# Optimization experiments

Measured on AMD Instinct MI355X. Metric: run time of the kernel, lower is better.

## Reference

```python
import jax, jax.numpy as jnp
import numpy as np

EMBED_DIM = 1024
NUM_HEADS = 16
HEAD_DIM = EMBED_DIM // NUM_HEADS
MAX_LEN = 1000  # default in RelativePositionalEncoding
B, T = 4, 1024


def setup_inputs() -> dict:
    key = jax.random.key(0)
    ks = jax.random.split(key, 12)
    s = 0.02
    d = EMBED_DIM
    return {
        "query": jax.random.normal(ks[0], (B, T, d), jnp.float32),
        "key": jax.random.normal(ks[1], (B, T, d), jnp.float32),
        "value": jax.random.normal(ks[2], (B, T, d), jnp.float32),
        "Wq": jax.random.normal(ks[3], (d, d), jnp.float32) * s,
        "bq": jnp.zeros((d,), jnp.float32),
        "Wk": jax.random.normal(ks[4], (d, d), jnp.float32) * s,
        "bk": jnp.zeros((d,), jnp.float32),
        "Wv": jax.random.normal(ks[5], (d, d), jnp.float32) * s,
        "bv": jnp.zeros((d,), jnp.float32),
        "Wo": jax.random.normal(ks[6], (d, d), jnp.float32) * s,
        "bo": jnp.zeros((d,), jnp.float32),
        "rel_emb": jax.random.normal(ks[7], (2 * MAX_LEN - 1, HEAD_DIM), jnp.float32) * s,
    }


def reference(query, key, value, Wq, bq, Wk, bk, Wv, bv, Wo, bo, rel_emb):
    Bq, Tq, C = query.shape
    H, hd = NUM_HEADS, HEAD_DIM
    # projections -> [B, H, T, hd]
    q = (query @ Wq.T + bq).reshape(Bq, Tq, H, hd).transpose(0, 2, 1, 3)
    k = (key @ Wk.T + bk).reshape(Bq, Tq, H, hd).transpose(0, 2, 1, 3)
    v = (value @ Wv.T + bv).reshape(Bq, Tq, H, hd).transpose(0, 2, 1, 3)
    # content scores [B, H, T, T]
    attn_scores = jnp.einsum('bhtd,bhsd->bhts', q, k)
    # relative positional embedding gather: E[t, s] = rel_emb[clamp(s - t + max_len - 1)]
    pos = jnp.arange(Tq)
    idx = jnp.clip(pos[None, :] - pos[:, None] + MAX_LEN - 1, 0, 2 * MAX_LEN - 2)
    E = rel_emb[idx]  # [T, T, hd]
    # NOTE: original uses raw (unprojected) query reshaped into heads for rel-pos scores
    rpe_q = query.transpose(1, 0, 2).reshape(Tq, Bq * H, hd)  # [T, B*H, hd]
    rpe = jnp.einsum('tnd,tsd->nts', rpe_q, E).reshape(Bq, H, Tq, Tq)
    # faithful to original: divide by scale = hd**-0.5 (i.e. multiply by sqrt(hd))
    scale = hd ** (-0.5)
    attn = (attn_scores + rpe) / scale
    attn_weights = jax.nn.softmax(attn, axis=-1)
    out = jnp.einsum('bhts,bhsd->bhtd', attn_weights, v)
    out = out.transpose(0, 2, 1, 3).reshape(Bq, Tq, C)
    return out @ Wo.T + bo
```

## Files before the change

kernel.cpp:

```cpp
#include <hip/hip_runtime.h>
#include <math.h>

typedef _Float16 h16;
typedef __attribute__((ext_vector_type(4))) _Float16 half4;
typedef __attribute__((ext_vector_type(8))) _Float16 half8;
typedef __attribute__((ext_vector_type(4))) float f32x4;

#define AS1 __attribute__((address_space(1)))
#define AS3 __attribute__((address_space(3)))
#define MFMA16(a, b, c) __builtin_amdgcn_mfma_f32_16x16x32_f16((a), (b), (c), 0, 0, 0)

__device__ __forceinline__ float ex2(float x) {
  return __builtin_amdgcn_exp2f(x);
}

__global__ __launch_bounds__(256) void convert(
    const float* __restrict__ q, const float* __restrict__ k,
    const float* __restrict__ v, const float* __restrict__ Wq,
    const float* __restrict__ Wk, const float* __restrict__ Wv,
    const float* __restrict__ Wo, const float* __restrict__ rel, h16* q16c,
    h16* k16c, h16* v16c, h16* Wq16, h16* Wk16, h16* Wv16, h16* Wo16,
    h16* relb) {
  const int i = blockIdx.x * 256 + threadIdx.x;
  if (i >= 4226304) return;
  const float* src;
  h16* dst;
  int off;
  if (i < 1048576) {
    src = q; dst = q16c; off = i;
  } else if (i < 2097152) {
    src = k; dst = k16c; off = i - 1048576;
  } else if (i < 3145728) {
    src = v; dst = v16c; off = i - 2097152;
  } else if (i < 3407872) {
    src = Wq; dst = Wq16; off = i - 3145728;
  } else if (i < 3670016) {
    src = Wk; dst = Wk16; off = i - 3407872;
  } else if (i < 3932160) {
    src = Wv; dst = Wv16; off = i - 3670016;
  } else if (i < 4194304) {
    src = Wo; dst = Wo16; off = i - 3932160;
  } else {
    off = i - 4194304;
    half4 hv = (half4){(h16)0.f, (h16)0.f, (h16)0.f, (h16)0.f};
    if (off < 31984) {
      float4 f = *(const float4*)(rel + (size_t)off * 4);
      hv = (half4){(h16)f.x, (h16)f.y, (h16)f.z, (h16)f.w};
    }
    *(half4*)(relb + (size_t)off * 4) = hv;
    return;
  }
  float4 f = *(const float4*)(src + (size_t)off * 4);
  *(half4*)(dst + (size_t)off * 4) =
      (half4){(h16)f.x, (h16)f.y, (h16)f.z, (h16)f.w};
}

template <int MODE>
__device__ __forceinline__ void gemm128_body(const h16* __restrict__ A,
                                             const h16* __restrict__ Bt,
                                             const float* __restrict__ bias,
                                             h16* __restrict__ outp) {
  __shared__ alignas(16) h16 As[128 * 32];
  __shared__ alignas(16) h16 Bs[128 * 32];
  const int tid = threadIdx.x;
  const int wave = tid >> 6;
  const int lane = tid & 63;
  const int wm = wave >> 1, wn = wave & 1;
  const int tm0 = blockIdx.x * 128, tn0 = blockIdx.y * 128;
  const int lrow = lane & 15;
  const int kq = lane >> 4;
  const int srow = lane >> 2;
  const int scol = (lane & 3) * 8;

  f32x4 acc[4][4];
#pragma unroll
  for (int i = 0; i < 4; ++i)
#pragma unroll
    for (int j = 0; j < 4; ++j) acc[i][j] = (f32x4){0.f, 0.f, 0.f, 0.f};

  for (int k0 = 0; k0 < 1024; k0 += 32) {
    __syncthreads();
#pragma unroll
    for (int rep = 0; rep < 2; ++rep) {
      const int cw = wave * 2 + rep;
      const int row = cw * 16 + srow;
      __builtin_amdgcn_global_load_lds(
          (const AS1 void*)(A + (size_t)(tm0 + row) * 1024 + k0 + scol),
          (AS3 void*)(As + cw * 512), 16, 0, 0);
      __builtin_amdgcn_global_load_lds(
          (const AS1 void*)(Bt + (size_t)(tn0 + row) * 1024 + k0 + scol),
          (AS3 void*)(Bs + cw * 512), 16, 0, 0);
    }
    __syncthreads();
    half8 af[4], bf[4];
#pragma unroll
    for (int i = 0; i < 4; ++i)
      af[i] = *(const half8*)(As + (wm * 64 + i * 16 + lrow) * 32 + kq * 8);
#pragma unroll
    for (int j = 0; j < 4; ++j)
      bf[j] = *(const half8*)(Bs + (wn * 64 + j * 16 + lrow) * 32 + kq * 8);
#pragma unroll
    for (int i = 0; i < 4; ++i)
#pragma unroll
      for (int j = 0; j < 4; ++j) acc[i][j] = MFMA16(af[i], bf[j], acc[i][j]);
  }

#pragma unroll
  for (int j = 0; j < 4; ++j) {
    const int n = tn0 + wn * 64 + j * 16 + lrow;
    const float bval = bias[n];
#pragma unroll
    for (int i = 0; i < 4; ++i) {
      const int rowb = wm * 64 + i * 16 + kq * 4;
#pragma unroll
      for (int r = 0; r < 4; ++r) {
        const int m = tm0 + rowb + r;
        const float val = acc[i][j][r] + bval;
        const int b = m >> 10, t = m & 1023, hh = n >> 6, d = n & 63;
        if (MODE == 0) {
          outp[((size_t)((b << 4) + hh) << 16) + (t << 6) + d] = (h16)val;
        } else {
          outp[(((size_t)((b << 4) + hh) * 64 + d) << 10) + t] = (h16)val;
        }
      }
    }
  }
}

__global__ __launch_bounds__(256) void qkv_gemm(
    const h16* q16c, const h16* k16c, const h16* v16c, const h16* Wq16,
    const h16* Wk16, const h16* Wv16, const float* bq, const float* bk,
    const float* bv, h16* q16, h16* k16, h16* vt16) {
  const int z = blockIdx.z;
  const h16* A = (z == 0) ? q16c : (z == 1) ? k16c : v16c;
  const h16* Bt = (z == 0) ? Wq16 : (z == 1) ? Wk16 : Wv16;
  const float* bias = (z == 0) ? bq : (z == 1) ? bk : bv;
  if (z == 2)
    gemm128_body<1>(A, Bt, bias, vt16);
  else
    gemm128_body<0>(A, Bt, bias, (z == 0) ? q16 : k16);
}

__global__ __launch_bounds__(256) void out_gemm(const h16* __restrict__ A,
                                                const h16* __restrict__ Bt,
                                                const float* __restrict__ bo,
                                                float* __restrict__ out) {
  __shared__ alignas(16) h16 As[64 * 32];
  __shared__ alignas(16) h16 Bs[128 * 32];
  const int tid = threadIdx.x;
  const int wave = tid >> 6;
  const int lane = tid & 63;
  const int wm = wave >> 1, wn = wave & 1;
  const int tm0 = blockIdx.x * 64, tn0 = blockIdx.y * 128;
  const int lrow = lane & 15;
  const int kq = lane >> 4;
  const int srow = lane >> 2;
  const int scol = (lane & 3) * 8;

  f32x4 acc[2][4];
#pragma unroll
  for (int i = 0; i < 2; ++i)
#pragma unroll
    for (int j = 0; j < 4; ++j) acc[i][j] = (f32x4){0.f, 0.f, 0.f, 0.f};

  for (int k0 = 0; k0 < 1024; k0 += 32) {
    __syncthreads();
    {
      const int row = wave * 16 + srow;
      __builtin_amdgcn_global_load_lds(
          (const AS1 void*)(A + (size_t)(tm0 + row) * 1024 + k0 + scol),
          (AS3 void*)(As + wave * 512), 16, 0, 0);
    }
#pragma unroll
    for (int rep = 0; rep < 2; ++rep) {
      const int cw = wave * 2 + rep;
      const int row = cw * 16 + srow;
      __builtin_amdgcn_global_load_lds(
          (const AS1 void*)(Bt + (size_t)(tn0 + row) * 1024 + k0 + scol),
          (AS3 void*)(Bs + cw * 512), 16, 0, 0);
    }
    __syncthreads();
    half8 af[2], bf[4];
#pragma unroll
    for (int i = 0; i < 2; ++i)
      af[i] = *(const half8*)(As + (wm * 32 + i * 16 + lrow) * 32 + kq * 8);
#pragma unroll
    for (int j = 0; j < 4; ++j)
      bf[j] = *(const half8*)(Bs + (wn * 64 + j * 16 + lrow) * 32 + kq * 8);
#pragma unroll
    for (int i = 0; i < 2; ++i)
#pragma unroll
      for (int j = 0; j < 4; ++j) acc[i][j] = MFMA16(af[i], bf[j], acc[i][j]);
  }

#pragma unroll
  for (int j = 0; j < 4; ++j) {
    const int n = tn0 + wn * 64 + j * 16 + lrow;
    const float bval = bo[n];
#pragma unroll
    for (int i = 0; i < 2; ++i) {
      const int rowb = wm * 32 + i * 16 + kq * 4;
#pragma unroll
      for (int r = 0; r < 4; ++r) {
        const int m = tm0 + rowb + r;
        out[(size_t)m * 1024 + n] = acc[i][j][r] + bval;
      }
    }
  }
}

__global__ __launch_bounds__(256, 4) void attn_mfma(
    const h16* __restrict__ q16, const h16* __restrict__ k16,
    const h16* __restrict__ vt16, const h16* __restrict__ q16c,
    const h16* __restrict__ relb, h16* __restrict__ ao) {
  __shared__ alignas(16) h16 Kh[4096];
  __shared__ alignas(16) h16 Rl[8192];
  __shared__ alignas(16) h16 VtS[4096];
  __shared__ alignas(16) h16 Ps[4096];

  const int bid = blockIdx.x;
  const int ttile = bid & 15;
  const int bh = bid >> 4;
  const int b = bh >> 4, h = bh & 15;
  const int t0 = ttile << 6;
  const int tid = threadIdx.x;
  const int w = tid >> 6;
  const int lane = tid & 63;
  const int l15 = lane & 15;
  const int kq = lane >> 4;

  const int tq = t0 + w * 16 + l15;
  half8 aq[2], arq[2];
#pragma unroll
  for (int ks = 0; ks < 2; ++ks) {
    aq[ks] =
        *(const half8*)(q16 + ((size_t)bh * 1024 + tq) * 64 + kq * 8 + ks * 32);
    arq[ks] = *(const half8*)(q16c + ((size_t)(b * 1024 + tq)) * 1024 + h * 64 +
                              kq * 8 + ks * 32);
  }

  float m2[4], ls[4];
  f32x4 O[4];
#pragma unroll
  for (int r = 0; r < 4; ++r) {
    m2[r] = -1e30f;
    ls[r] = 0.f;
  }
#pragma unroll
  for (int db = 0; db < 4; ++db) O[db] = (f32x4){0.f, 0.f, 0.f, 0.f};

  const int trow = w * 16 + kq * 4;

  for (int s0 = 0; s0 < 1024; s0 += 64) {
    __syncthreads();
    for (int i = tid; i < 512; i += 256) {
      const int row = i >> 3, c = i & 7;
      *(half8*)(Kh + row * 64 + ((c ^ (row & 7)) << 3)) = *(const half8*)(
          k16 + ((size_t)(bh * 1024 + s0 + row)) * 64 + c * 8);
    }
    for (int i = tid; i < 512; i += 256) {
      const int row = i >> 3, c = i & 7;
      *(half8*)(VtS + row * 64 + ((c ^ (row & 7)) << 3)) = *(const half8*)(
          vt16 + ((size_t)bh * 64 + row) * 1024 + s0 + c * 8);
    }
    const int base = s0 - t0 + 999 - 63;
    for (int i = tid; i < 1024; i += 256) {
      const int row = i >> 3, c = i & 7;
      int ridx = base + row;
      ridx = ridx < 0 ? 0 : (ridx > 1998 ? 1998 : ridx);
      *(half8*)(Rl + row * 64 + ((c ^ (row & 7)) << 3)) =
          *(const half8*)(relb + (size_t)ridx * 64 + c * 8);
    }
    __syncthreads();

    f32x4 S[4];
#pragma unroll
    for (int ns = 0; ns < 4; ++ns) {
      f32x4 s = (f32x4){0.f, 0.f, 0.f, 0.f};
      const int kr = ns * 16 + l15;
#pragma unroll
      for (int ks = 0; ks < 2; ++ks) {
        const int c = ((ks * 4 + kq) ^ (kr & 7)) << 3;
        s = MFMA16(aq[ks], *(const half8*)(Kh + kr * 64 + c), s);
      }
      S[ns] = s;
    }

    f32x4 G[5];
#pragma unroll
    for (int gi = 0; gi < 5; ++gi) {
      f32x4 g = (f32x4){0.f, 0.f, 0.f, 0.f};
      const int ur = (3 - w + gi) * 16 + l15;
#pragma unroll
      for (int ks = 0; ks < 2; ++ks) {
        const int c = ((ks * 4 + kq) ^ (ur & 7)) << 3;
        g = MFMA16(arq[ks], *(const half8*)(Rl + ur * 64 + c), g);
      }
      G[gi] = g;
    }

    const float SC = 11.54156032711170727f;
    const int C0 = 63 - w * 16 - kq * 4;
#pragma unroll
    for (int ns = 0; ns < 4; ++ns) {
#pragma unroll
      for (int r = 0; r < 4; ++r) {
        const int u = l15 + C0 + ns * 16 - r;
        const int src = (kq << 4) | (u & 15);
        const int gsel = (u >> 4) + w - 3;
        const float v0 = __shfl(G[ns][r], src, 64);
        const float v1 = __shfl(G[(ns + 1) <= 4 ? (ns + 1) : 4][r], src, 64);
        const float g = (gsel == ns) ? v0 : v1;
        S[ns][r] = (S[ns][r] + g) * SC;
      }
    }

#pragma unroll
    for (int r = 0; r < 4; ++r) {
      float mx = fmaxf(fmaxf(S[0][r], S[1][r]), fmaxf(S[2][r], S[3][r]));
      mx = fmaxf(mx, __shfl_xor(mx, 1));
      mx = fmaxf(mx, __shfl_xor(mx, 2));
      mx = fmaxf(mx, __shfl_xor(mx, 4));
      mx = fmaxf(mx, __shfl_xor(mx, 8));
      const float nm = fmaxf(m2[r], mx);
      const float al = ex2(m2[r] - nm);
      m2[r] = nm;
      const int t = trow + r;
      float rs = 0.f;
#pragma unroll
      for (int ns = 0; ns < 4; ++ns) {
        const float p = ex2(S[ns][r] - nm);
        rs += p;
        const int sl = ns * 16 + l15;
        Ps[t * 64 + (((sl >> 3) ^ (t & 7)) << 3) + (sl & 7)] = (h16)p;
      }
      rs += __shfl_xor(rs, 1);
      rs += __shfl_xor(rs, 2);
      rs += __shfl_xor(rs, 4);
      rs += __shfl_xor(rs, 8);
      ls[r] = ls[r] * al + rs;
      O[0][r] *= al;
      O[1][r] *= al;
      O[2][r] *= al;
      O[3][r] *= al;
    }

    const int tp = w * 16 + l15;
#pragma unroll
    for (int ks = 0; ks < 2; ++ks) {
      const int ca = ((ks * 4 + kq) ^ (tp & 7)) << 3;
      half8 pa = *(const half8*)(Ps + tp * 64 + ca);
#pragma unroll
      for (int db = 0; db < 4; ++db) {
        const int vr = db * 16 + l15;
        const int cb = ((ks * 4 + kq) ^ (vr & 7)) << 3;
        O[db] = MFMA16(pa, *(const half8*)(VtS + vr * 64 + cb), O[db]);
      }
    }
  }

#pragma unroll
  for (int r = 0; r < 4; ++r) {
    const float inv = 1.f / ls[r];
    const int t = t0 + trow + r;
    h16* op = ao + ((size_t)(b * 1024 + t)) * 1024 + h * 64;
#pragma unroll
    for (int db = 0; db < 4; ++db) op[db * 16 + l15] = (h16)(O[db][r] * inv);
  }
}

extern "C" void kernel_launch(void* const* d_in, const int* in_sizes, int n_in,
                              void* d_out, int out_size, void* d_ws,
                              size_t ws_size, hipStream_t stream) {
  const float* query = (const float*)d_in[0];
  const float* key = (const float*)d_in[1];
  const float* value = (const float*)d_in[2];
  const float* Wq = (const float*)d_in[3];
  const float* bq = (const float*)d_in[4];
  const float* Wk = (const float*)d_in[5];
  const float* bk = (const float*)d_in[6];
  const float* Wv = (const float*)d_in[7];
  const float* bv = (const float*)d_in[8];
  const float* Wo = (const float*)d_in[9];
  const float* bo = (const float*)d_in[10];
  const float* rel = (const float*)d_in[11];

  char* ws = (char*)d_ws;
  h16* q16c = (h16*)ws;
  h16* k16c = (h16*)(ws + ((size_t)8 << 20));
  h16* v16c = (h16*)(ws + ((size_t)16 << 20));
  h16* Wq16 = (h16*)(ws + ((size_t)24 << 20));
  h16* Wk16 = (h16*)(ws + ((size_t)26 << 20));
  h16* Wv16 = (h16*)(ws + ((size_t)28 << 20));
  h16* Wo16 = (h16*)(ws + ((size_t)30 << 20));
  h16* q16 = (h16*)(ws + ((size_t)32 << 20));
  h16* k16 = (h16*)(ws + ((size_t)40 << 20));
  h16* vt16 = (h16*)(ws + ((size_t)48 << 20));
  h16* relb = (h16*)(ws + ((size_t)56 << 20));
  h16* ao = k16c;
  float* out = (float*)d_out;

  convert<<<16509, 256, 0, stream>>>(query, key, value, Wq, Wk, Wv, Wo, rel,
                                     q16c, k16c, v16c, Wq16, Wk16, Wv16, Wo16,
                                     relb);
  qkv_gemm<<<dim3(32, 8, 3), 256, 0, stream>>>(q16c, k16c, v16c, Wq16, Wk16,
                                               Wv16, bq, bk, bv, q16, k16,
                                               vt16);
  attn_mfma<<<1024, 256, 0, stream>>>(q16, k16, vt16, q16c, relb, ao);
  out_gemm<<<dim3(64, 8), 256, 0, stream>>>(ao, Wo16, bo, out);
}
```

Measured before the change: 288.2 us.

## Load K/V/rel fragments directly from global, vectorize GEMM epilogue stores, swizzle block order

The attention kernel stops staging K, V^T and relative-embedding tiles in shared memory and has each wave read its MFMA operands straight from global memory (L1/L2), which removes two barriers per iteration and most of the LDS footprint. Block indices are remapped so that consecutive blocks cover different heads for the same t-tile, changing L2 locality for the rel-embedding reads. The QKV GEMM swaps the MFMA operand order in Q/K mode so that each lane holds four contiguous output columns, allowing half4 stores and a float4 bias load instead of scalar scattered stores. Each wave now re-reads K/V from global memory instead of sharing one staged copy, which depends on cache hit rates.

New measurement: 363.0 us. +26.0%, slower.

```diff
diff --git a/kernel.cpp b/kernel.cpp
--- a/kernel.cpp
+++ b/kernel.cpp
@@ -102,26 +102,42 @@
 #pragma unroll
     for (int i = 0; i < 4; ++i)
 #pragma unroll
-      for (int j = 0; j < 4; ++j) acc[i][j] = MFMA16(af[i], bf[j], acc[i][j]);
-  }
-
-#pragma unroll
-  for (int j = 0; j < 4; ++j) {
-    const int n = tn0 + wn * 64 + j * 16 + lrow;
-    const float bval = bias[n];
+      for (int j = 0; j < 4; ++j) {
+        if (MODE == 0)
+          acc[i][j] = MFMA16(bf[j], af[i], acc[i][j]);
+        else
+          acc[i][j] = MFMA16(af[i], bf[j], acc[i][j]);
+      }
+  }
+
+  if (MODE == 0) {
 #pragma unroll
     for (int i = 0; i < 4; ++i) {
-      const int rowb = wm * 64 + i * 16 + kq * 4;
-#pragma unroll
-      for (int r = 0; r < 4; ++r) {
-        const int m = tm0 + rowb + r;
-        const float val = acc[i][j][r] + bval;
-        const int b = m >> 10, t = m & 1023, hh = n >> 6, d = n & 63;
-        if (MODE == 0) {
-          outp[((size_t)((b << 4) + hh) << 16) + (t << 6) + d] = (h16)val;
-        } else {
-          outp[(((size_t)((b << 4) + hh) * 64 + d) << 10) + t] = (h16)val;
-        }
+      const int m = tm0 + wm * 64 + i * 16 + lrow;
+      const int b = m >> 10, t = m & 1023;
+#pragma unroll
+      for (int j = 0; j < 4; ++j) {
+        const int n0 = tn0 + wn * 64 + j * 16 + kq * 4;
+        const float4 bv = *(const float4*)(bias + n0);
+        const int hh = n0 >> 6, d0 = n0 & 63;
+        half4 hv = (half4){(h16)(acc[i][j][0] + bv.x), (h16)(acc[i][j][1] + bv.y),
+                           (h16)(acc[i][j][2] + bv.z), (h16)(acc[i][j][3] + bv.w)};
+        *(half4*)(outp + ((size_t)((b << 4) + hh) << 16) + (t << 6) + d0) = hv;
+      }
+    }
+  } else {
+#pragma unroll
+    for (int j = 0; j < 4; ++j) {
+      const int n = tn0 + wn * 64 + j * 16 + lrow;
+      const float bval = bias[n];
+      const int hh = n >> 6, d = n & 63;
+#pragma unroll
+      for (int i = 0; i < 4; ++i) {
+        const int m0 = tm0 + wm * 64 + i * 16 + kq * 4;
+        const int b = m0 >> 10, t = m0 & 1023;
+        half4 hv = (half4){(h16)(acc[i][j][0] + bval), (h16)(acc[i][j][1] + bval),
+                           (h16)(acc[i][j][2] + bval), (h16)(acc[i][j][3] + bval)};
+        *(half4*)(outp + (((size_t)((b << 4) + hh) * 64 + d) << 10) + t) = hv;
       }
     }
   }
@@ -213,14 +229,11 @@
     const h16* __restrict__ q16, const h16* __restrict__ k16,
     const h16* __restrict__ vt16, const h16* __restrict__ q16c,
     const h16* __restrict__ relb, h16* __restrict__ ao) {
-  __shared__ alignas(16) h16 Kh[4096];
-  __shared__ alignas(16) h16 Rl[8192];
-  __shared__ alignas(16) h16 VtS[4096];
   __shared__ alignas(16) h16 Ps[4096];
 
-  const int bid = blockIdx.x;
-  const int ttile = bid & 15;
-  const int bh = bid >> 4;
+  const int i0 = blockIdx.x;
+  const int bh = ((i0 & 7) << 3) | (i0 >> 7);
+  const int ttile = (i0 >> 3) & 15;
   const int b = bh >> 4, h = bh & 15;
   const int t0 = ttile << 6;
   const int tid = threadIdx.x;
@@ -234,9 +247,9 @@
 #pragma unroll
   for (int ks = 0; ks < 2; ++ks) {
     aq[ks] =
-        *(const half8*)(q16 + ((size_t)bh * 1024 + tq) * 64 + kq * 8 + ks * 32);
+        *(const half8*)(q16 + ((size_t)bh * 1024 + tq) * 64 + ks * 32 + kq * 8);
     arq[ks] = *(const half8*)(q16c + ((size_t)(b * 1024 + tq)) * 1024 + h * 64 +
-                              kq * 8 + ks * 32);
+                              ks * 32 + kq * 8);
   }
 
   float m2[4], ls[4];
@@ -250,52 +263,35 @@
   for (int db = 0; db < 4; ++db) O[db] = (f32x4){0.f, 0.f, 0.f, 0.f};
 
   const int trow = w * 16 + kq * 4;
+  const h16* kbh = k16 + ((size_t)bh << 10) * 64;
+  const h16* vbh = vt16 + ((size_t)bh << 6) * 1024;
 
   for (int s0 = 0; s0 < 1024; s0 += 64) {
-    __syncthreads();
-    for (int i = tid; i < 512; i += 256) {
-      const int row = i >> 3, c = i & 7;
-      *(half8*)(Kh + row * 64 + ((c ^ (row & 7)) << 3)) = *(const half8*)(
-          k16 + ((size_t)(bh * 1024 + s0 + row)) * 64 + c * 8);
-    }
-    for (int i = tid; i < 512; i += 256) {
-      const int row = i >> 3, c = i & 7;
-      *(half8*)(VtS + row * 64 + ((c ^ (row & 7)) << 3)) = *(const half8*)(
-          vt16 + ((size_t)bh * 64 + row) * 1024 + s0 + c * 8);
-    }
-    const int base = s0 - t0 + 999 - 63;
-    for (int i = tid; i < 1024; i += 256) {
-      const int row = i >> 3, c = i & 7;
-      int ridx = base + row;
-      ridx = ridx < 0 ? 0 : (ridx > 1998 ? 1998 : ridx);
-      *(half8*)(Rl + row * 64 + ((c ^ (row & 7)) << 3)) =
-          *(const half8*)(relb + (size_t)ridx * 64 + c * 8);
-    }
-    __syncthreads();
-
     f32x4 S[4];
 #pragma unroll
     for (int ns = 0; ns < 4; ++ns) {
       f32x4 s = (f32x4){0.f, 0.f, 0.f, 0.f};
-      const int kr = ns * 16 + l15;
-#pragma unroll
-      for (int ks = 0; ks < 2; ++ks) {
-        const int c = ((ks * 4 + kq) ^ (kr & 7)) << 3;
-        s = MFMA16(aq[ks], *(const half8*)(Kh + kr * 64 + c), s);
-      }
+      const int kr = s0 + ns * 16 + l15;
+#pragma unroll
+      for (int ks = 0; ks < 2; ++ks)
+        s = MFMA16(aq[ks],
+                   *(const half8*)(kbh + (size_t)kr * 64 + ks * 32 + kq * 8), s);
       S[ns] = s;
     }
 
+    const int base = s0 - t0 + 936;
     f32x4 G[5];
 #pragma unroll
     for (int gi = 0; gi < 5; ++gi) {
       f32x4 g = (f32x4){0.f, 0.f, 0.f, 0.f};
       const int ur = (3 - w + gi) * 16 + l15;
-#pragma unroll
-      for (int ks = 0; ks < 2; ++ks) {
-        const int c = ((ks * 4 + kq) ^ (ur & 7)) << 3;
-        g = MFMA16(arq[ks], *(const half8*)(Rl + ur * 64 + c), g);
-      }
+      int ridx = base + ur;
+      ridx = ridx < 0 ? 0 : (ridx > 1998 ? 1998 : ridx);
+#pragma unroll
+      for (int ks = 0; ks < 2; ++ks)
+        g = MFMA16(arq[ks],
+                   *(const half8*)(relb + (size_t)ridx * 64 + ks * 32 + kq * 8),
+                   g);
       G[gi] = g;
     }
 
@@ -353,8 +349,10 @@
 #pragma unroll
       for (int db = 0; db < 4; ++db) {
         const int vr = db * 16 + l15;
-        const int cb = ((ks * 4 + kq) ^ (vr & 7)) << 3;
-        O[db] = MFMA16(pa, *(const half8*)(VtS + vr * 64 + cb), O[db]);
+        O[db] = MFMA16(
+            pa,
+            *(const half8*)(vbh + (size_t)vr * 1024 + s0 + ks * 32 + kq * 8),
+            O[db]);
       }
     }
   }
```
